# Optimization experiments

Measured on AMD Instinct MI355X. Metric: run time of the kernel, lower is better.

The kernel has to match this reference:

```python
import jax, jax.numpy as jnp
import numpy as np

BETA = 0.2
ALPHA_NEG = 0.8
ALPHA_POS = 0.2
EPS = 1e-8  # torch cosine_similarity eps

B, D, P = 8192, 256, 4096


def setup_inputs() -> dict:
    key = jax.random.key(0)
    k1, k2 = jax.random.split(key)
    embeddings = jax.random.normal(k1, (B, D), dtype=jnp.float32)
    positive_pairs = jax.random.randint(k2, (P, 2), 0, B, dtype=jnp.int32)
    return {"embeddings": embeddings, "positive_pairs": positive_pairs}


def reference(embeddings, positive_pairs):
    b = embeddings.shape[0]
    p = positive_pairs.shape[0]
    # cosine similarity matrix (normalize once, single GEMM)
    nrm = jnp.maximum(jnp.linalg.norm(embeddings, axis=1, keepdims=True), EPS)
    e = embeddings / nrm
    cos = e @ e.T                              # [B, B]
    exp_cos = jnp.exp(cos / BETA)
    ii = positive_pairs[:, 0]
    jj = positive_pairs[:, 1]
    # mask = eye + positive pairs (both directions)
    mask = jnp.eye(b, dtype=bool)
    mask = mask.at[ii, jj].set(True).at[jj, ii].set(True)
    exp_masked = jnp.where(mask, 0.0, exp_cos)  # masked_fill(mask, 0)
    pos_ij = exp_cos[ii, jj]                   # [P]
    pos_ji = exp_cos[jj, ii]                   # [P]
    exp_i = exp_masked[ii]                     # [P, B]
    exp_j = exp_masked[jj]                     # [P, B]
    # hard-negative mining via alpha_neg quantile per row
    thr_i = jnp.quantile(exp_i, ALPHA_NEG, axis=1, keepdims=True)
    thr_j = jnp.quantile(exp_j, ALPHA_NEG, axis=1, keepdims=True)
    S_i = jnp.sum(jnp.where(exp_i >= thr_i, exp_i, 0.0), axis=1)  # [P]
    S_j = jnp.sum(jnp.where(exp_j >= thr_j, exp_j, 0.0), axis=1)  # [P]
    # hard-positive mining via alpha_pos quantile
    thr_pij = jnp.quantile(pos_ij, ALPHA_POS)
    thr_pji = jnp.quantile(pos_ji, ALPHA_POS)
    sel_ij = pos_ij <= thr_pij
    sel_ji = pos_ji <= thr_pji
    # torch loop zips the two (order-preserving) boolean-selected lists ->
    # truncates to min count; values are never cross-coupled, only the count.
    kmin = jnp.minimum(sel_ij.sum(), sel_ji.sum())
    act_ij = sel_ij & ((jnp.cumsum(sel_ij.astype(jnp.int32)) - 1) < kmin)
    act_ji = sel_ji & ((jnp.cumsum(sel_ji.astype(jnp.int32)) - 1) < kmin)
    # -log(pk / (pk + S[m])) = log1p(S[m] / pk), summed over all m per pk
    term_ij = jnp.log1p(S_i[None, :] / pos_ij[:, None])  # [P, P]
    term_ji = jnp.log1p(S_j[None, :] / pos_ji[:, None])  # [P, P]
    loss = (jnp.sum(term_ij * act_ij[:, None].astype(term_ij.dtype))
            + jnp.sum(term_ji * act_ji[:, None].astype(term_ji.dtype)))
    return loss / (2.0 * p)
```

## Files before the change

kernel.cpp:

```cpp
#include <hip/hip_runtime.h>
#include <stdint.h>

#define BN    8192
#define DK    256
#define PN    4096
#define MAXP  16
#define RANK_ASC 6553
#define QSTEP 0.02f

typedef float f32x4  __attribute__((ext_vector_type(4)));
typedef int   i32x4  __attribute__((ext_vector_type(4)));

__device__ __forceinline__ void gload_lds16(const void* g, void* l) {
  __builtin_amdgcn_global_load_lds(
      (const __attribute__((address_space(1))) unsigned int*)g,
      (__attribute__((address_space(3))) unsigned int*)l, 16, 0, 0);
}

__device__ __forceinline__ void find_bin_256(const unsigned* hist, int rank,
                                             int* sh, unsigned* wtot) {
  const int tid = threadIdx.x, lane = tid & 63, w = tid >> 6;
  unsigned x = hist[tid];
  unsigned pref = x;
  #pragma unroll
  for (int o = 1; o < 64; o <<= 1) {
    unsigned y = __shfl_up(pref, o);
    if (lane >= o) pref += y;
  }
  if (lane == 63) wtot[w] = pref;
  __syncthreads();
  unsigned woff = 0;
  for (int i = 0; i < w; ++i) woff += wtot[i];
  unsigned incl = pref + woff, excl = incl - x;
  if ((unsigned)rank >= excl && (unsigned)rank < incl) { sh[0] = tid; sh[1] = rank - (int)excl; }
  __syncthreads();
}

__device__ __forceinline__ float block_sum4(float x, float* red4) {
  const int lane = threadIdx.x & 63, w = threadIdx.x >> 6;
  #pragma unroll
  for (int o = 32; o; o >>= 1) x += __shfl_xor(x, o);
  __syncthreads();
  if (lane == 0) red4[w] = x;
  __syncthreads();
  return red4[0] + red4[1] + red4[2] + red4[3];
}

__global__ void __launch_bounds__(256) norm_pairs_kernel(
    const float* __restrict__ X, float* __restrict__ E, signed char* __restrict__ Ei8,
    const int2* __restrict__ pairs, int* pcount, int* partners) {
  const int tid  = threadIdx.x;
  const int lane = tid & 63;
  const int wib  = tid >> 6;
  const int row  = blockIdx.x * 4 + wib;

  float4 x = ((const float4*)(X + (size_t)row * DK))[lane];
  float ss = x.x * x.x + x.y * x.y + x.z * x.z + x.w * x.w;
  #pragma unroll
  for (int o = 32; o; o >>= 1) ss += __shfl_xor(ss, o);
  float nrm = fmaxf(sqrtf(ss), 1e-8f);
  float4 e;
  e.x = x.x / nrm; e.y = x.y / nrm; e.z = x.z / nrm; e.w = x.w / nrm;
  ((float4*)(E + (size_t)row * DK))[lane] = e;
  int c0 = (int)rintf(127.0f * e.x);
  int c1 = (int)rintf(127.0f * e.y);
  int c2 = (int)rintf(127.0f * e.z);
  int c3 = (int)rintf(127.0f * e.w);
  unsigned u = (unsigned)(c0 & 255) | ((unsigned)(c1 & 255) << 8)
             | ((unsigned)(c2 & 255) << 16) | ((unsigned)(c3 & 255) << 24);
  ((unsigned*)(Ei8 + (size_t)row * DK))[lane] = u;

  const int p = blockIdx.x * 256 + tid;
  if (p < PN) {
    int2 pr = pairs[p];
    int ix = atomicAdd(&pcount[pr.x], 1);
    if (ix < MAXP) partners[pr.x * MAXP + ix] = pr.y;
    int iy = atomicAdd(&pcount[pr.y], 1);
    if (iy < MAXP) partners[pr.y * MAXP + iy] = pr.x;
  }
}

__global__ void __launch_bounds__(256) compact_pos_kernel(
    const int* __restrict__ pcount, int* rowlist, int* cnt,
    const float* __restrict__ E, const int2* __restrict__ pairs,
    float* __restrict__ pos) {
  const int tid  = threadIdx.x;
  const int lane = tid & 63;
  const int wib  = tid >> 6;
  const int gix  = blockIdx.x * 256 + tid;

  if (gix < BN && pcount[gix] > 0) {
    int ppos = atomicAdd(cnt, 1);
    rowlist[ppos] = gix;
  }

  const int p = blockIdx.x * 4 + wib;
  int2 pr = pairs[p];
  float4 a = ((const float4*)(E + (size_t)pr.x * DK))[lane];
  float4 b = ((const float4*)(E + (size_t)pr.y * DK))[lane];
  float d = a.x * b.x + a.y * b.y + a.z * b.z + a.w * b.w;
  #pragma unroll
  for (int o = 32; o; o >>= 1) d += __shfl_xor(d, o);
  if (lane == 0) pos[p] = __expf(5.0f * d);
}

__global__ void __launch_bounds__(256) gemm_code_kernel(
    const signed char* __restrict__ Ei8, const int* __restrict__ rowlist,
    const int* __restrict__ countp, uint32_t* __restrict__ out4) {
  if ((int)blockIdx.y * 128 >= *countp) return;
  __shared__ __align__(16) signed char sA[128 * 64];
  __shared__ __align__(16) signed char sB[128 * 64];
  const int tid  = threadIdx.x;
  const int lane = tid & 63;
  const int w    = tid >> 6;
  const int wm   = w >> 1, wn = w & 1;
  const int trow = blockIdx.y * 128;
  const int tcol = blockIdx.x * 128;

  const int r0  = tid >> 2;
  const int r1  = 64 + r0;
  const int sl_ = tid & 3;
  const int sg0 = sl_ ^ ((r0 >> 1) & 3);
  const int sg1 = sl_ ^ ((r1 >> 1) & 3);
  const int ga0 = rowlist[trow + r0];
  const int ga1 = rowlist[trow + r1];
  const signed char* pa0 = Ei8 + (size_t)ga0 * DK + sg0 * 16;
  const signed char* pa1 = Ei8 + (size_t)ga1 * DK + sg1 * 16;
  const signed char* pb0 = Ei8 + (size_t)(tcol + r0) * DK + sg0 * 16;
  const signed char* pb1 = Ei8 + (size_t)(tcol + r1) * DK + sg1 * 16;
  signed char* la0 = &sA[tid * 16];
  signed char* la1 = &sA[4096 + tid * 16];
  signed char* lb0 = &sB[tid * 16];
  signed char* lb1 = &sB[4096 + tid * 16];

  i32x4 acc[4][4];
  #pragma unroll
  for (int i = 0; i < 4; ++i)
    #pragma unroll
    for (int j = 0; j < 4; ++j) {
      i32x4 z = {0, 0, 0, 0};
      acc[i][j] = z;
    }

  const int g = lane >> 4;
  for (int kt = 0; kt < 4; ++kt) {
    const int k0 = kt * 64;
    __syncthreads();
    gload_lds16(pa0 + k0, la0);
    gload_lds16(pa1 + k0, la1);
    gload_lds16(pb0 + k0, lb0);
    gload_lds16(pb1 + k0, lb1);
    __syncthreads();
    i32x4 af[4], bfg[4];
    #pragma unroll
    for (int q = 0; q < 4; ++q) {
      const int ra = wm * 64 + q * 16 + (lane & 15);
      const int rb = wn * 64 + q * 16 + (lane & 15);
      af[q]  = *(const i32x4*)&sA[ra * 64 + (g ^ ((ra >> 1) & 3)) * 16];
      bfg[q] = *(const i32x4*)&sB[rb * 64 + (g ^ ((rb >> 1) & 3)) * 16];
    }
    #pragma unroll
    for (int i = 0; i < 4; ++i)
      #pragma unroll
      for (int j = 0; j < 4; ++j)
        acc[i][j] = __builtin_amdgcn_mfma_i32_16x16x64_i8(af[i], bfg[j], acc[i][j], 0, 0, 0);
  }

  const int crow = trow + wm * 64 + (lane >> 4) * 4;
  const int ccol = tcol + wn * 64 + (lane & 15);
  const float SCL = 250.0f / 16129.0f;
  #pragma unroll
  for (int i = 0; i < 4; ++i) {
    const int gidx = (crow + i * 16) >> 2;
    #pragma unroll
    for (int j = 0; j < 4; ++j) {
      const int col = ccol + j * 16;
      uint32_t u = 0;
      #pragma unroll
      for (int r = 0; r < 4; ++r) {
        int c = (int)fmaf((float)acc[i][j][r], SCL, 128.5f);
        c = c < 1 ? 1 : (c > 255 ? 255 : c);
        u |= (uint32_t)c << (8 * r);
      }
      out4[(size_t)gidx * BN + col] = u;
    }
  }
}

__global__ void __launch_bounds__(256) row_stats4_kernel(
    const uint32_t* __restrict__ expc4, const int* __restrict__ rowlist,
    const int* __restrict__ countp, const int* __restrict__ pcount,
    const int* __restrict__ partners, float* __restrict__ S) {
  __shared__ unsigned hist[4][4][256];
  __shared__ unsigned total[4][256];
  __shared__ int plist[4][MAXP + 1];
  __shared__ int npl[4];
  __shared__ int growl[4];
  __shared__ int sh[2];
  __shared__ unsigned wtot[4];
  __shared__ float redf[4];
  const int g = blockIdx.x;
  const int cnt = *countp;
  if (g * 4 >= cnt) return;
  const int tid = threadIdx.x, lane = tid & 63, w = tid >> 6;

  uint4 rv[8];
  const uint4* src = (const uint4*)(expc4 + (size_t)g * BN);
  #pragma unroll
  for (int q = 0; q < 8; ++q) rv[q] = src[q * 256 + tid];

  if (tid < 4) {
    int rr = g * 4 + tid;
    int grow = (rr < cnt) ? rowlist[rr] : -1;
    growl[tid] = grow;
    int np = 0;
    if (grow >= 0) {
      np = pcount[grow]; if (np > MAXP) np = MAXP;
      for (int e = 0; e < np; ++e) plist[tid][e] = partners[grow * MAXP + e];
      plist[tid][np] = grow;
      np++;
    }
    npl[tid] = np;
  }
  #pragma unroll
  for (int k = 0; k < 16; ++k) ((unsigned*)hist)[k * 256 + tid] = 0;
  __syncthreads();

  #pragma unroll
  for (int r4 = 0; r4 < 4; ++r4) {
    const int np = npl[r4];
    for (int e = 0; e < np; ++e) {
      int c = plist[r4][e];
      int t = c >> 2;
      if ((t & 255) == tid) {
        unsigned* wp = (unsigned*)&rv[t >> 8];
        wp[c & 3] &= ~(0xFFu << (r4 * 8));
      }
    }
  }

  unsigned* h = (unsigned*)hist[w];
  #pragma unroll
  for (int q = 0; q < 8; ++q) {
    #pragma unroll
    for (int word = 0; word < 4; ++word) {
      unsigned dw = ((const unsigned*)&rv[q])[word];
      atomicAdd(&h[0 * 256 + (dw & 255u)], 1u);
      atomicAdd(&h[1 * 256 + ((dw >> 8) & 255u)], 1u);
      atomicAdd(&h[2 * 256 + ((dw >> 16) & 255u)], 1u);
      atomicAdd(&h[3 * 256 + (dw >> 24)], 1u);
    }
  }
  __syncthreads();
  #pragma unroll
  for (int r4 = 0; r4 < 4; ++r4)
    total[r4][tid] = hist[0][r4][tid] + hist[1][r4][tid] + hist[2][r4][tid] + hist[3][r4][tid];
  __syncthreads();

  const float val = __expf((float)(tid - 128) * QSTEP);
  for (int r4 = 0; r4 < 4; ++r4) {
    find_bin_256(total[r4], RANK_ASC, sh, wtot);
    const int b    = sh[0];
    const int need = (int)total[r4][b] - sh[1];
    float contrib = (tid > b) ? (float)total[r4][tid] * val
                  : (tid == b) ? (float)need * val : 0.f;
    #pragma unroll
    for (int o = 32; o; o >>= 1) contrib += __shfl_xor(contrib, o);
    __syncthreads();
    if (lane == 0) redf[w] = contrib;
    __syncthreads();
    if (tid == 0 && growl[r4] >= 0)
      S[growl[r4]] = redf[0] + redf[1] + redf[2] + redf[3];
    __syncthreads();
  }
}

__global__ void __launch_bounds__(256) finale_kernel(
    const float* __restrict__ pos, const int2* __restrict__ pairs,
    const float* __restrict__ S, float* __restrict__ out) {
  __shared__ uint32_t v[PN];
  __shared__ unsigned hist[256];
  __shared__ int sh[2];
  __shared__ unsigned wtot[4];
  __shared__ float red4[4];
  const int tid = threadIdx.x;
  for (int i = tid; i < PN; i += 256) v[i] = ((const uint32_t*)pos)[i];
  __syncthreads();
  int rank = 819;
  uint32_t prefix = 0;
  for (int pass = 0; pass < 4; ++pass) {
    const int shift = 24 - pass * 8;
    hist[tid] = 0;
    __syncthreads();
    for (int i = tid; i < PN; i += 256) {
      uint32_t x = v[i];
      bool match = (pass == 0) || ((x >> (shift + 8)) == (prefix >> (shift + 8)));
      if (match) atomicAdd(&hist[(x >> shift) & 255u], 1u);
    }
    __syncthreads();
    find_bin_256(hist, rank, sh, wtot);
    prefix |= ((uint32_t)sh[0]) << shift;
    rank = sh[1];
    __syncthreads();
  }
  float thr; __builtin_memcpy(&thr, &prefix, 4);

  float n = 0.f, sl = 0.f, sp = 0.f, sp2 = 0.f;
  for (int r = tid; r < PN; r += 256) {
    float p; uint32_t b = v[r]; __builtin_memcpy(&p, &b, 4);
    if (p <= thr) { n += 1.f; sl += __logf(p); sp += p; sp2 += p * p; }
  }
  float t = 0.f, u = 0.f, vv = 0.f;
  for (int c = tid; c < PN; c += 256) {
    int2 pr = pairs[c];
    float s1 = S[pr.x], s2 = S[pr.y];
    float i1 = 1.f / s1, i2 = 1.f / s2;
    t += __logf(s1) + __logf(s2);
    u += i1 + i2;
    vv += i1 * i1 + i2 * i2;
  }
  const float N   = block_sum4(n, red4);
  const float SL  = block_sum4(sl, red4);
  const float SP  = block_sum4(sp, red4);
  const float SP2 = block_sum4(sp2, red4);
  const float T   = block_sum4(t, red4);
  const float U   = block_sum4(u, red4);
  const float V   = block_sum4(vv, red4);
  if (tid == 0) {
    double num = (double)N * T - 2.0 * (double)PN * (double)SL
               + (double)SP * U - 0.5 * (double)SP2 * V;
    out[0] = (float)(num / (2.0 * (double)PN));
  }
}

extern "C" void kernel_launch(void* const* d_in, const int* in_sizes, int n_in,
                              void* d_out, int out_size, void* d_ws, size_t ws_size,
                              hipStream_t stream) {
  const float* emb  = (const float*)d_in[0];
  const int2* pairs = (const int2*)d_in[1];
  float* out = (float*)d_out;

  char* w = (char*)d_ws;
  size_t off = 0;
  int*         pcnt  = (int*)(w + off);         off += (size_t)BN * 4;
  int*         rlist = (int*)(w + off);         off += (size_t)BN * 4;
  int*         cnt   = (int*)(w + off);         off += 256;
  float*       E     = (float*)(w + off);       off += (size_t)BN * DK * 4;
  signed char* Ei8   = (signed char*)(w + off); off += (size_t)BN * DK;
  float*       S     = (float*)(w + off);       off += (size_t)BN * 4;
  float*       pos   = (float*)(w + off);       off += (size_t)PN * 4;
  int*         parts = (int*)(w + off);         off += (size_t)BN * MAXP * 4;
  uint32_t*    out4  = (uint32_t*)(w + off);    off += (size_t)(BN / 4) * BN * 4;

  hipMemsetAsync(pcnt, 0, (size_t)BN * 8 + 256, stream);
  norm_pairs_kernel<<<BN / 4, 256, 0, stream>>>(emb, E, Ei8, pairs, pcnt, parts);
  compact_pos_kernel<<<PN / 4, 256, 0, stream>>>(pcnt, rlist, cnt, E, pairs, pos);
  gemm_code_kernel<<<dim3(BN / 128, BN / 128), 256, 0, stream>>>(Ei8, rlist, cnt, out4);
  row_stats4_kernel<<<BN / 4, 256, 0, stream>>>(out4, rlist, cnt, pcnt, parts, S);
  finale_kernel<<<1, 256, 0, stream>>>(pos, pairs, S, out);
}
```

Before: 152.2 us.

## Drop fp32 normalized buffer, build rowlist via atomics, widen GEMM K-tile

The normalize kernel no longer writes an fp32 normalized copy. It writes only int8 codes and builds the active-row list directly, recording a row the first time its pair counter is incremented. Positive-pair similarities are now computed from the int8 codes instead of fp32, which cuts memory traffic but makes pos values depend on the quantization. The GEMM uses a 128-wide K tile with 8-way XOR swizzle, halving the number of barrier-separated load phases, and the row list order becomes nondeterministic.

```diff
diff --git a/kernel.cpp b/kernel.cpp
--- a/kernel.cpp
+++ b/kernel.cpp
@@ -47,8 +47,9 @@
 }
 
 __global__ void __launch_bounds__(256) norm_pairs_kernel(
-    const float* __restrict__ X, float* __restrict__ E, signed char* __restrict__ Ei8,
-    const int2* __restrict__ pairs, int* pcount, int* partners) {
+    const float* __restrict__ X, signed char* __restrict__ Ei8,
+    const int2* __restrict__ pairs, int* pcount, int* partners,
+    int* rowlist, int* cnt) {
   const int tid  = threadIdx.x;
   const int lane = tid & 63;
   const int wib  = tid >> 6;
@@ -58,14 +59,11 @@
   float ss = x.x * x.x + x.y * x.y + x.z * x.z + x.w * x.w;
   #pragma unroll
   for (int o = 32; o; o >>= 1) ss += __shfl_xor(ss, o);
-  float nrm = fmaxf(sqrtf(ss), 1e-8f);
-  float4 e;
-  e.x = x.x / nrm; e.y = x.y / nrm; e.z = x.z / nrm; e.w = x.w / nrm;
-  ((float4*)(E + (size_t)row * DK))[lane] = e;
-  int c0 = (int)rintf(127.0f * e.x);
-  int c1 = (int)rintf(127.0f * e.y);
-  int c2 = (int)rintf(127.0f * e.z);
-  int c3 = (int)rintf(127.0f * e.w);
+  float inv = 127.0f / fmaxf(sqrtf(ss), 1e-8f);
+  int c0 = (int)rintf(inv * x.x);
+  int c1 = (int)rintf(inv * x.y);
+  int c2 = (int)rintf(inv * x.z);
+  int c3 = (int)rintf(inv * x.w);
   unsigned u = (unsigned)(c0 & 255) | ((unsigned)(c1 & 255) << 8)
              | ((unsigned)(c2 & 255) << 16) | ((unsigned)(c3 & 255) << 24);
   ((unsigned*)(Ei8 + (size_t)row * DK))[lane] = u;
@@ -74,42 +72,42 @@
   if (p < PN) {
     int2 pr = pairs[p];
     int ix = atomicAdd(&pcount[pr.x], 1);
+    if (ix == 0) { int q = atomicAdd(cnt, 1); rowlist[q] = pr.x; }
     if (ix < MAXP) partners[pr.x * MAXP + ix] = pr.y;
     int iy = atomicAdd(&pcount[pr.y], 1);
+    if (iy == 0) { int q = atomicAdd(cnt, 1); rowlist[q] = pr.y; }
     if (iy < MAXP) partners[pr.y * MAXP + iy] = pr.x;
   }
 }
 
-__global__ void __launch_bounds__(256) compact_pos_kernel(
-    const int* __restrict__ pcount, int* rowlist, int* cnt,
-    const float* __restrict__ E, const int2* __restrict__ pairs,
+__global__ void __launch_bounds__(256) pos_kernel(
+    const signed char* __restrict__ Ei8, const int2* __restrict__ pairs,
     float* __restrict__ pos) {
   const int tid  = threadIdx.x;
   const int lane = tid & 63;
   const int wib  = tid >> 6;
-  const int gix  = blockIdx.x * 256 + tid;
-
-  if (gix < BN && pcount[gix] > 0) {
-    int ppos = atomicAdd(cnt, 1);
-    rowlist[ppos] = gix;
-  }
-
-  const int p = blockIdx.x * 4 + wib;
+  const int p    = blockIdx.x * 4 + wib;
   int2 pr = pairs[p];
-  float4 a = ((const float4*)(E + (size_t)pr.x * DK))[lane];
-  float4 b = ((const float4*)(E + (size_t)pr.y * DK))[lane];
-  float d = a.x * b.x + a.y * b.y + a.z * b.z + a.w * b.w;
-  #pragma unroll
-  for (int o = 32; o; o >>= 1) d += __shfl_xor(d, o);
-  if (lane == 0) pos[p] = __expf(5.0f * d);
+  int a = ((const int*)(Ei8 + (size_t)pr.x * DK))[lane];
+  int b = ((const int*)(Ei8 + (size_t)pr.y * DK))[lane];
+  int s = 0;
+  #pragma unroll
+  for (int j = 0; j < 4; ++j) {
+    int va = (int)(signed char)(a >> (8 * j));
+    int vb = (int)(signed char)(b >> (8 * j));
+    s += va * vb;
+  }
+  #pragma unroll
+  for (int o = 32; o; o >>= 1) s += __shfl_xor(s, o);
+  if (lane == 0) pos[p] = __expf((float)s * (5.0f / 16129.0f));
 }
 
 __global__ void __launch_bounds__(256) gemm_code_kernel(
     const signed char* __restrict__ Ei8, const int* __restrict__ rowlist,
     const int* __restrict__ countp, uint32_t* __restrict__ out4) {
   if ((int)blockIdx.y * 128 >= *countp) return;
-  __shared__ __align__(16) signed char sA[128 * 64];
-  __shared__ __align__(16) signed char sB[128 * 64];
+  __shared__ __align__(16) signed char sA[128 * 128];
+  __shared__ __align__(16) signed char sB[128 * 128];
   const int tid  = threadIdx.x;
   const int lane = tid & 63;
   const int w    = tid >> 6;
@@ -117,21 +115,15 @@
   const int trow = blockIdx.y * 128;
   const int tcol = blockIdx.x * 128;
 
-  const int r0  = tid >> 2;
-  const int r1  = 64 + r0;
-  const int sl_ = tid & 3;
-  const int sg0 = sl_ ^ ((r0 >> 1) & 3);
-  const int sg1 = sl_ ^ ((r1 >> 1) & 3);
-  const int ga0 = rowlist[trow + r0];
-  const int ga1 = rowlist[trow + r1];
-  const signed char* pa0 = Ei8 + (size_t)ga0 * DK + sg0 * 16;
-  const signed char* pa1 = Ei8 + (size_t)ga1 * DK + sg1 * 16;
-  const signed char* pb0 = Ei8 + (size_t)(tcol + r0) * DK + sg0 * 16;
-  const signed char* pb1 = Ei8 + (size_t)(tcol + r1) * DK + sg1 * 16;
-  signed char* la0 = &sA[tid * 16];
-  signed char* la1 = &sA[4096 + tid * 16];
-  signed char* lb0 = &sB[tid * 16];
-  signed char* lb1 = &sB[4096 + tid * 16];
+  const int srow = tid >> 3;
+  const int sl   = tid & 7;
+  const int sg   = sl ^ (srow & 7);
+  int garow[4], gbrow[4];
+  #pragma unroll
+  for (int ii = 0; ii < 4; ++ii) {
+    garow[ii] = rowlist[trow + ii * 32 + srow];
+    gbrow[ii] = tcol + ii * 32 + srow;
+  }
 
   i32x4 acc[4][4];
   #pragma unroll
@@ -142,28 +134,32 @@
       acc[i][j] = z;
     }
 
-  const int g = lane >> 4;
-  for (int kt = 0; kt < 4; ++kt) {
-    const int k0 = kt * 64;
-    __syncthreads();
-    gload_lds16(pa0 + k0, la0);
-    gload_lds16(pa1 + k0, la1);
-    gload_lds16(pb0 + k0, lb0);
-    gload_lds16(pb1 + k0, lb1);
-    __syncthreads();
-    i32x4 af[4], bfg[4];
-    #pragma unroll
-    for (int q = 0; q < 4; ++q) {
-      const int ra = wm * 64 + q * 16 + (lane & 15);
-      const int rb = wn * 64 + q * 16 + (lane & 15);
-      af[q]  = *(const i32x4*)&sA[ra * 64 + (g ^ ((ra >> 1) & 3)) * 16];
-      bfg[q] = *(const i32x4*)&sB[rb * 64 + (g ^ ((rb >> 1) & 3)) * 16];
-    }
-    #pragma unroll
-    for (int i = 0; i < 4; ++i)
+  for (int kt = 0; kt < 2; ++kt) {
+    const int k0 = kt * 128;
+    __syncthreads();
+    #pragma unroll
+    for (int ii = 0; ii < 4; ++ii) {
+      gload_lds16(Ei8 + (size_t)garow[ii] * DK + k0 + sg * 16, &sA[ii * 4096 + tid * 16]);
+      gload_lds16(Ei8 + (size_t)gbrow[ii] * DK + k0 + sg * 16, &sB[ii * 4096 + tid * 16]);
+    }
+    __syncthreads();
+    #pragma unroll
+    for (int h = 0; h < 2; ++h) {
+      const int fg = h * 4 + (lane >> 4);
+      i32x4 af[4], bfg[4];
       #pragma unroll
-      for (int j = 0; j < 4; ++j)
-        acc[i][j] = __builtin_amdgcn_mfma_i32_16x16x64_i8(af[i], bfg[j], acc[i][j], 0, 0, 0);
+      for (int q = 0; q < 4; ++q) {
+        const int ra = wm * 64 + q * 16 + (lane & 15);
+        const int rb = wn * 64 + q * 16 + (lane & 15);
+        af[q]  = *(const i32x4*)&sA[ra * 128 + (fg ^ (ra & 7)) * 16];
+        bfg[q] = *(const i32x4*)&sB[rb * 128 + (fg ^ (rb & 7)) * 16];
+      }
+      #pragma unroll
+      for (int i = 0; i < 4; ++i)
+        #pragma unroll
+        for (int j = 0; j < 4; ++j)
+          acc[i][j] = __builtin_amdgcn_mfma_i32_16x16x64_i8(af[i], bfg[j], acc[i][j], 0, 0, 0);
+    }
   }
 
   const int crow = trow + wm * 64 + (lane >> 4) * 4;
@@ -345,7 +341,6 @@
   int*         pcnt  = (int*)(w + off);         off += (size_t)BN * 4;
   int*         rlist = (int*)(w + off);         off += (size_t)BN * 4;
   int*         cnt   = (int*)(w + off);         off += 256;
-  float*       E     = (float*)(w + off);       off += (size_t)BN * DK * 4;
   signed char* Ei8   = (signed char*)(w + off); off += (size_t)BN * DK;
   float*       S     = (float*)(w + off);       off += (size_t)BN * 4;
   float*       pos   = (float*)(w + off);       off += (size_t)PN * 4;
@@ -353,8 +348,8 @@
   uint32_t*    out4  = (uint32_t*)(w + off);    off += (size_t)(BN / 4) * BN * 4;
 
   hipMemsetAsync(pcnt, 0, (size_t)BN * 8 + 256, stream);
-  norm_pairs_kernel<<<BN / 4, 256, 0, stream>>>(emb, E, Ei8, pairs, pcnt, parts);
-  compact_pos_kernel<<<PN / 4, 256, 0, stream>>>(pcnt, rlist, cnt, E, pairs, pos);
+  norm_pairs_kernel<<<BN / 4, 256, 0, stream>>>(emb, Ei8, pairs, pcnt, parts, rlist, cnt);
+  pos_kernel<<<PN / 4, 256, 0, stream>>>(Ei8, pairs, pos);
   gemm_code_kernel<<<dim3(BN / 128, BN / 128), 256, 0, stream>>>(Ei8, rlist, cnt, out4);
   row_stats4_kernel<<<BN / 4, 256, 0, stream>>>(out4, rlist, cnt, pcnt, parts, S);
   finale_kernel<<<1, 256, 0, stream>>>(pos, pairs, S, out);
```

Result: faster. 148.3 us, median of 2 (-2.6%).
